# Kernel optimization log

Measured on AMD Instinct MI355X. Metric: run time of the kernel, lower is better.

The kernel has to match this reference:

```python
import jax, jax.numpy as jnp
import numpy as np

N_HEADS = 16
N_KV_HEADS = 4
HEAD_DIM = 64
ROPE_BASE = 10000.0

def _rope_cos_sin(T, dtype):
    # flash-attn style: cos/sin of shape [T, head_dim//2]
    inv_freq = 1.0 / (ROPE_BASE ** (jnp.arange(0, HEAD_DIM, 2, dtype=jnp.float32) / HEAD_DIM))
    freqs = jnp.arange(T, dtype=jnp.float32)[:, None] * inv_freq[None, :]  # [T, D/2]
    return jnp.cos(freqs).astype(dtype), jnp.sin(freqs).astype(dtype)

def _apply_rope(x, cos, sin):
    # x: [B, H, T, D], non-interleaved rotate-half on full head dim
    d2 = HEAD_DIM // 2
    x1, x2 = x[..., :d2], x[..., d2:]
    c = cos[None, None, :, :]
    s = sin[None, None, :, :]
    return jnp.concatenate([x1 * c - x2 * s, x2 * c + x1 * s], axis=-1)

def setup_inputs() -> dict:
    key = jax.random.key(0)
    ks = jax.random.split(key, 6)
    B, T, D = 1, 4096, 1024
    def g(k, shape, scale):
        return jax.random.normal(k, shape, dtype=jnp.float32) * scale
    return {
        "query": g(ks[0], (B, T, D), 1.0),
        "Wq": g(ks[1], (D, D), D ** -0.5),
        "Wk": g(ks[2], (D, N_KV_HEADS * HEAD_DIM), D ** -0.5),
        "Wv": g(ks[3], (D, N_KV_HEADS * HEAD_DIM), D ** -0.5),
        "W1": g(ks[4], (D, 4 * D), D ** -0.5),
        "W2": g(ks[5], (4 * D, D), (4 * D) ** -0.5),
    }

def reference(query, Wq, Wk, Wv, W1, W2):
    B, T, D = query.shape
    # QKV projections -> [B, H, T, Dh]
    q = (query @ Wq).reshape(B, T, N_HEADS, HEAD_DIM).transpose(0, 2, 1, 3)
    k = (query @ Wk).reshape(B, T, N_KV_HEADS, HEAD_DIM).transpose(0, 2, 1, 3)
    v = (query @ Wv).reshape(B, T, N_KV_HEADS, HEAD_DIM).transpose(0, 2, 1, 3)
    # RoPE (seqlen_offset = 0, no cache)
    cos, sin = _rope_cos_sin(T, q.dtype)
    q = _apply_rope(q, cos, sin)
    k = _apply_rope(k, cos, sin)
    # GQA: repeat KV heads to match Q heads
    n_rep = N_HEADS // N_KV_HEADS
    k = jnp.repeat(k, n_rep, axis=1)
    v = jnp.repeat(v, n_rep, axis=1)
    # Scaled dot-product attention, causal
    scale = HEAD_DIM ** -0.5
    scores = jnp.einsum("bhqd,bhkd->bhqk", q, k) * scale
    i = jnp.arange(T)[:, None]
    j = jnp.arange(T)[None, :]
    scores = jnp.where(j > i, jnp.finfo(scores.dtype).min, scores)
    attn = jax.nn.softmax(scores, axis=-1)
    out = jnp.einsum("bhqk,bhkd->bhqd", attn, v)  # [B, H, T, Dh]
    out = out.transpose(0, 2, 1, 3).reshape(B, T, D)
    # out_proj: Linear -> SiLU -> Linear (use_swiglu=True path)
    return jax.nn.silu(out @ W1) @ W2
```

## Files before the change

### kernel.cpp

```cpp
#include <hip/hip_runtime.h>
#include <stdint.h>

typedef unsigned short u16;
typedef __bf16 bf16x8 __attribute__((ext_vector_type(8)));
typedef float f32x4 __attribute__((ext_vector_type(4)));

#define T_SEQ 4096
#define DMODEL 1024

__device__ __forceinline__ float bf2f(u16 x) {
  union { uint32_t u; float f; } v; v.u = ((uint32_t)x) << 16; return v.f;
}
__device__ __forceinline__ u16 f2bf(float f) {
  union { float f; uint32_t u; } v; v.f = f;
  return (u16)((v.u + 0x7FFFu + ((v.u >> 16) & 1u)) >> 16);
}
__device__ __forceinline__ float fexp2(float x) {
#if __has_builtin(__builtin_amdgcn_exp2f)
  return __builtin_amdgcn_exp2f(x);
#else
  return __expf(x * 0.6931471805599453f);
#endif
}
__device__ __forceinline__ uint32_t pack_bf16(float lo, float hi) {
#if __has_builtin(__builtin_amdgcn_cvt_pk_bf16_f32)
  typedef __bf16 bf16x2_t __attribute__((ext_vector_type(2)));
  union { bf16x2_t v; uint32_t u; } c;
  c.v = __builtin_amdgcn_cvt_pk_bf16_f32(lo, hi);
  return c.u;
#else
  union { float f; uint32_t u; } a, b;
  a.f = lo; b.f = hi;
  return __builtin_amdgcn_perm(b.u + 0x8000u, a.u + 0x8000u, 0x07060302u);
#endif
}
__device__ __forceinline__ void async16(void* lds, const void* g) {
  __builtin_amdgcn_global_load_lds(
      (__attribute__((address_space(1))) void*)const_cast<void*>(g),
      (__attribute__((address_space(3))) void*)lds, 16, 0, 0);
}
__device__ __forceinline__ void storeC(u16* C, size_t i, float v) { C[i] = f2bf(v); }
__device__ __forceinline__ void storeC(float* C, size_t i, float v) { C[i] = v; }

__global__ void __launch_bounds__(256) f2b_copy(const float* __restrict__ in,
                                                u16* __restrict__ out, int n) {
  int idx = (blockIdx.x * 256 + threadIdx.x) * 4;
  if (idx >= n) return;
  float4 v = *(const float4*)(in + idx);
  union { u16 s[4]; uint2 q; } b;
  b.s[0] = f2bf(v.x); b.s[1] = f2bf(v.y); b.s[2] = f2bf(v.z); b.s[3] = f2bf(v.w);
  *(uint2*)(out + idx) = b.q;
}

__global__ void __launch_bounds__(256) wtrans(const float* __restrict__ in,
                                              u16* __restrict__ out, int K, int N) {
  __shared__ float tile[64][65];
  const int n0 = blockIdx.x * 64, k0 = blockIdx.y * 64;
  const int tid = threadIdx.x;
  const int r = tid >> 2, c = (tid & 3) * 16;
#pragma unroll
  for (int j = 0; j < 4; ++j) {
    float4 v = *(const float4*)&in[(size_t)(k0 + r) * N + n0 + c + j * 4];
    tile[r][c + j * 4 + 0] = v.x; tile[r][c + j * 4 + 1] = v.y;
    tile[r][c + j * 4 + 2] = v.z; tile[r][c + j * 4 + 3] = v.w;
  }
  __syncthreads();
  union { u16 s[16]; uint4 q[2]; } buf;
#pragma unroll
  for (int j = 0; j < 16; ++j) buf.s[j] = f2bf(tile[c + j][r]);
  u16* dst = out + (size_t)(n0 + r) * K + k0 + c;
  *(uint4*)(dst) = buf.q[0];
  *(uint4*)(dst + 8) = buf.q[1];
}

__global__ void __launch_bounds__(256) vtrans(const u16* __restrict__ qkv,
                                              u16* __restrict__ Vt) {
  __shared__ u16 tile[64][65];
  const int t0 = blockIdx.x * 64, h = blockIdx.y;
  const int tid = threadIdx.x;
  const int r = tid >> 2, q4 = (tid & 3) * 16;
  const u16* src = qkv + (size_t)(t0 + r) * 1536 + 1280 + h * 64 + q4;
  union { u16 s[16]; uint4 q[2]; } buf;
  buf.q[0] = *(const uint4*)(src);
  buf.q[1] = *(const uint4*)(src + 8);
#pragma unroll
  for (int j = 0; j < 16; ++j) tile[r][q4 + j] = buf.s[j];
  __syncthreads();
#pragma unroll
  for (int j = 0; j < 16; ++j) buf.s[j] = tile[q4 + j][r];
  u16* dst = Vt + ((size_t)h * 64 + r) * T_SEQ + t0 + q4;
  *(uint4*)(dst) = buf.q[0];
  *(uint4*)(dst + 8) = buf.q[1];
}

__global__ void __launch_bounds__(256) rope_qk(const u16* __restrict__ qkv,
                                               u16* __restrict__ Q, u16* __restrict__ Ko) {
  const int t = blockIdx.x;
  const int tid = threadIdx.x;
  const int i = tid & 31;
  const float ang = (float)t * powf(10000.f, -(float)i * (1.f / 32.f));
  float s, c;
  sincosf(ang, &s, &c);
  const u16* row = qkv + (size_t)t * 1536;
  const float QS = 0.125f * 1.4426950408889634f;
  const float cq = c * QS, sq = s * QS;
#pragma unroll
  for (int it = 0; it < 2; ++it) {
    int h = (tid >> 5) + it * 8;
    float x1 = bf2f(row[h * 64 + i]);
    float x2 = bf2f(row[h * 64 + 32 + i]);
    size_t o = ((size_t)h * T_SEQ + t) * 64 + i;
    Q[o] = f2bf(x1 * cq - x2 * sq);
    Q[o + 32] = f2bf(x2 * cq + x1 * sq);
  }
  if (tid < 128) {
    int h = tid >> 5;
    float x1 = bf2f(row[1024 + h * 64 + i]);
    float x2 = bf2f(row[1024 + h * 64 + 32 + i]);
    size_t o = ((size_t)h * T_SEQ + t) * 64 + i;
    Ko[o] = f2bf(x1 * c - x2 * s);
    Ko[o + 32] = f2bf(x2 * c + x1 * s);
  }
}

template <int AM, int ACT, typename OutT>
__global__ void __launch_bounds__(256) gemm_bt(const u16* __restrict__ A,
                                               const u16* __restrict__ Bt,
                                               OutT* __restrict__ C,
                                               int M, int N, int K) {
  __shared__ u16 sA[AM * 32][64];
  __shared__ u16 sB[128][64];
  const int tid = threadIdx.x;
  const int w = tid >> 6, lane = tid & 63;
  const int g = lane >> 4, l15 = lane & 15;
  const int r8 = lane >> 3, c8 = lane & 7;
  const int bm = blockIdx.y * (AM * 32), bn = blockIdx.x * 128;

  f32x4 acc[AM][4];
#pragma unroll
  for (int i = 0; i < AM; ++i)
#pragma unroll
    for (int j = 0; j < 4; ++j) acc[i][j] = (f32x4){0.f, 0.f, 0.f, 0.f};

  const u16* Ag = A + (size_t)(bm + w * (AM * 8) + r8) * K + (c8 ^ r8) * 8;
  const u16* Bg = Bt + (size_t)(bn + w * 32 + r8) * K + (c8 ^ r8) * 8;
  const int mrow = (w >> 1) * (AM * 16), ncol = (w & 1) * 64;
  const int swz = l15 & 7;

  for (int k0 = 0; k0 < K; k0 += 64) {
#pragma unroll
    for (int t = 0; t < AM; ++t)
      async16(&sA[w * (AM * 8) + t * 8][0], Ag + (size_t)(t * 8) * K + k0);
#pragma unroll
    for (int t = 0; t < 4; ++t)
      async16(&sB[w * 32 + t * 8][0], Bg + (size_t)(t * 8) * K + k0);
    __syncthreads();
#pragma unroll
    for (int kk = 0; kk < 2; ++kk) {
      const int cb = ((kk * 4 + g) ^ swz) * 8;
      bf16x8 a[AM], b[4];
#pragma unroll
      for (int i = 0; i < AM; ++i) a[i] = *(const bf16x8*)&sA[mrow + i * 16 + l15][cb];
#pragma unroll
      for (int i = 0; i < 4; ++i) b[i] = *(const bf16x8*)&sB[ncol + i * 16 + l15][cb];
#pragma unroll
      for (int mi = 0; mi < AM; ++mi)
#pragma unroll
        for (int ni = 0; ni < 4; ++ni)
          acc[mi][ni] = __builtin_amdgcn_mfma_f32_16x16x32_bf16(a[mi], b[ni], acc[mi][ni], 0, 0, 0);
    }
    __syncthreads();
  }
#pragma unroll
  for (int mi = 0; mi < AM; ++mi)
#pragma unroll
    for (int ni = 0; ni < 4; ++ni)
#pragma unroll
      for (int r = 0; r < 4; ++r) {
        int row = bm + mrow + mi * 16 + g * 4 + r;
        int col = bn + ncol + ni * 16 + l15;
        float v = acc[mi][ni][r];
        if (ACT == 1) v = v / (1.f + __expf(-v));
        storeC(C, (size_t)row * N + col, v);
      }
}

__global__ void __launch_bounds__(256, 2) attn(const u16* __restrict__ Q,
                                               const u16* __restrict__ K,
                                               const u16* __restrict__ Vt,
                                               u16* __restrict__ O0,
                                               u16* __restrict__ O1,
                                               float* __restrict__ L0,
                                               float* __restrict__ L1) {
  __shared__ u16 sK[2][64][64];
  __shared__ u16 sV[2][64][64];
  __shared__ u16 sP[4][64][68];
  const int pr = blockIdx.x >> 1;
  const int split = blockIdx.x & 1;
  const int h = blockIdx.y;
  const int kvh = h >> 2;
  const int tid = threadIdx.x;
  const int w = tid >> 6, lane = tid & 63;
  const int g = lane >> 4, l15 = lane & 15;
  const int r8 = lane >> 3, c8 = lane & 7;
  const int swz = l15 & 7;
  const int t0 = pr, t1 = 31 - pr;
  const int off = split * 64;

  u16* Op = split ? O1 : O0;
  float* Lp = split ? L1 : L0;

  bf16x8 qf[2][2][2];
  {
    const u16* Qh = Q + (size_t)h * T_SEQ * 64;
#pragma unroll
    for (int half = 0; half < 2; ++half)
#pragma unroll
      for (int mi = 0; mi < 2; ++mi) {
        const int q = (half ? t1 : t0) * 128 + w * 32 + mi * 16 + l15;
#pragma unroll
        for (int kk = 0; kk < 2; ++kk)
          qf[half][mi][kk] = *(const bf16x8*)(Qh + (size_t)q * 64 + (kk * 4 + g) * 8);
      }
  }

  f32x4 oacc[2][2][4];
  f32x4 lacc[2][2];
#pragma unroll
  for (int half = 0; half < 2; ++half)
#pragma unroll
    for (int mi = 0; mi < 2; ++mi) {
      lacc[half][mi] = (f32x4){0.f, 0.f, 0.f, 0.f};
#pragma unroll
      for (int nd = 0; nd < 4; ++nd) oacc[half][mi][nd] = (f32x4){0.f, 0.f, 0.f, 0.f};
    }

  bf16x8 ONES;
  {
    union { u16 s[8]; bf16x8 v; } o;
#pragma unroll
    for (int i = 0; i < 8; ++i) o.s[i] = 0x3F80;
    ONES = o.v;
  }

  const u16* Kg = K + ((size_t)kvh * T_SEQ + w * 16 + r8) * 64 + (c8 ^ r8) * 8;
  const u16* Vg = Vt + ((size_t)kvh * 64 + w * 16 + r8) * T_SEQ + (c8 ^ r8) * 8;

#define STAGE(J, B)                                                     \
  {                                                                     \
    const int kv0_ = (J) * 64;                                          \
    async16(&sK[B][w * 16 + 0][0], Kg + (size_t)kv0_ * 64);             \
    async16(&sK[B][w * 16 + 8][0], Kg + (size_t)(kv0_ + 8) * 64);       \
    async16(&sV[B][w * 16 + 0][0], Vg + kv0_);                          \
    async16(&sV[B][w * 16 + 8][0], Vg + (size_t)8 * T_SEQ + kv0_);      \
  }

#define BODY(B, ACT0, M0, M1)                                                     \
  {                                                                               \
    const int b_ = (B);                                                           \
    f32x4 s1[2][4], s0[2][4];                                                     \
    _Pragma("unroll") for (int mi = 0; mi < 2; ++mi)                              \
    _Pragma("unroll") for (int kt = 0; kt < 4; ++kt) {                            \
      s1[mi][kt] = (f32x4){0.f, 0.f, 0.f, 0.f};                                   \
      if (ACT0) s0[mi][kt] = (f32x4){0.f, 0.f, 0.f, 0.f};                         \
    }                                                                             \
    _Pragma("unroll") for (int kt = 0; kt < 4; ++kt)                              \
    _Pragma("unroll") for (int kk = 0; kk < 2; ++kk) {                            \
      bf16x8 kf = *(const bf16x8*)&sK[b_][kt * 16 + l15][((kk * 4 + g) ^ swz) * 8]; \
      _Pragma("unroll") for (int mi = 0; mi < 2; ++mi) {                          \
        s1[mi][kt] = __builtin_amdgcn_mfma_f32_16x16x32_bf16(kf, qf[1][mi][kk], s1[mi][kt], 0, 0, 0); \
        if (ACT0)                                                                 \
          s0[mi][kt] = __builtin_amdgcn_mfma_f32_16x16x32_bf16(kf, qf[0][mi][kk], s0[mi][kt], 0, 0, 0); \
      }                                                                           \
    }                                                                             \
    _Pragma("unroll") for (int mi = 0; mi < 2; ++mi) {                            \
      const int thr_ = w * 32 + mi * 16 + l15 - off;                              \
      _Pragma("unroll") for (int kt = 0; kt < 4; ++kt) {                          \
        float p_[4];                                                              \
        _Pragma("unroll") for (int r = 0; r < 4; ++r) {                           \
          float p = fexp2(s1[mi][kt][r]);                                         \
          if (M1 && (kt * 16 + g * 4 + r > thr_)) p = 0.f;                        \
          p_[r] = p;                                                              \
        }                                                                         \
        uint2 pk;                                                                 \
        pk.x = pack_bf16(p_[0], p_[1]);                                           \
        pk.y = pack_bf16(p_[2], p_[3]);                                           \
        *(uint2*)&sP[w][32 + mi * 16 + l15][kt * 16 + g * 4] = pk;                \
      }                                                                           \
      if (ACT0) {                                                                 \
        _Pragma("unroll") for (int kt = 0; kt < 4; ++kt) {                        \
          float p_[4];                                                            \
          _Pragma("unroll") for (int r = 0; r < 4; ++r) {                         \
            float p = fexp2(s0[mi][kt][r]);                                       \
            if (M0 && (kt * 16 + g * 4 + r > thr_)) p = 0.f;                      \
            p_[r] = p;                                                            \
          }                                                                       \
          uint2 pk;                                                               \
          pk.x = pack_bf16(p_[0], p_[1]);                                         \
          pk.y = pack_bf16(p_[2], p_[3]);                                         \
          *(uint2*)&sP[w][mi * 16 + l15][kt * 16 + g * 4] = pk;                   \
        }                                                                         \
      }                                                                           \
    }                                                                             \
    __builtin_amdgcn_wave_barrier();          \
    _Pragma("unroll") for (int kk = 0; kk < 2; ++kk) {                            \
      bf16x8 pf1[2], pf0[2];                                                      \
      _Pragma("unroll") for (int mi = 0; mi < 2; ++mi) {                          \
        pf1[mi] = *(const bf16x8*)&sP[w][32 + mi * 16 + l15][kk * 32 + g * 8];    \
        if (ACT0) pf0[mi] = *(const bf16x8*)&sP[w][mi * 16 + l15][kk * 32 + g * 8]; \
      }                                                                           \
      _Pragma("unroll") for (int mi = 0; mi < 2; ++mi) {                          \
        lacc[1][mi] = __builtin_amdgcn_mfma_f32_16x16x32_bf16(pf1[mi], ONES, lacc[1][mi], 0, 0, 0); \
        if (ACT0)                                                                 \
          lacc[0][mi] = __builtin_amdgcn_mfma_f32_16x16x32_bf16(pf0[mi], ONES, lacc[0][mi], 0, 0, 0); \
      }                                                                           \
      _Pragma("unroll") for (int nd = 0; nd < 4; ++nd) {                          \
        bf16x8 vf = *(const bf16x8*)&sV[b_][nd * 16 + l15][((kk * 4 + g) ^ swz) * 8]; \
        _Pragma("unroll") for (int mi = 0; mi < 2; ++mi) {                        \
          oacc[1][mi][nd] = __builtin_amdgcn_mfma_f32_16x16x32_bf16(pf1[mi], vf, oacc[1][mi][nd], 0, 0, 0); \
          if (ACT0)                                                               \
            oacc[0][mi][nd] = __builtin_amdgcn_mfma_f32_16x16x32_bf16(pf0[mi], vf, oacc[0][mi][nd], 0, 0, 0); \
        }                                                                         \
      }                                                                           \
    }                                                                             \
  }

  const int e0 = 2 * t0 + split, e1 = 2 * t1 + split;
  STAGE(split, 0);
  int jj = split, b = 0;
  for (; jj < e0; jj += 2, b ^= 1) {
    __syncthreads();
    STAGE(jj + 2, b ^ 1);
    BODY(b, true, false, false);
  }
  {
    __syncthreads();
    STAGE(jj + 2, b ^ 1);
    BODY(b, true, true, false);
    jj += 2; b ^= 1;
  }
  for (; jj < e1; jj += 2, b ^= 1) {
    __syncthreads();
    STAGE(jj + 2, b ^ 1);
    BODY(b, false, false, false);
  }
  {
    __syncthreads();
    BODY(b, false, false, true);
  }
#undef STAGE
#undef BODY

#pragma unroll
  for (int half = 0; half < 2; ++half) {
    const int tb = (half ? t1 : t0) * 128;
#pragma unroll
    for (int mi = 0; mi < 2; ++mi)
#pragma unroll
      for (int r = 0; r < 4; ++r) {
        const int trow = tb + w * 32 + mi * 16 + g * 4 + r;
#pragma unroll
        for (int nd = 0; nd < 4; ++nd)
          Op[(size_t)trow * DMODEL + h * 64 + nd * 16 + l15] = f2bf(oacc[half][mi][nd][r]);
        if (l15 == 0) Lp[h * T_SEQ + trow] = lacc[half][mi][r];
      }
  }
}

__global__ void __launch_bounds__(256) attn_combine(const u16* __restrict__ O0,
                                                    const u16* __restrict__ O1,
                                                    const float* __restrict__ L0,
                                                    const float* __restrict__ L1,
                                                    u16* __restrict__ AO) {
  const int t = blockIdx.x, tid = threadIdx.x;
  const int h = tid >> 4, d4 = (tid & 15) * 4;
  const float inv = 1.f / (L0[h * T_SEQ + t] + L1[h * T_SEQ + t]);
  const size_t idx = (size_t)t * DMODEL + h * 64 + d4;
  union { uint2 q; u16 s[4]; } a, b, o;
  a.q = *(const uint2*)(O0 + idx);
  b.q = *(const uint2*)(O1 + idx);
#pragma unroll
  for (int i = 0; i < 4; ++i) o.s[i] = f2bf((bf2f(a.s[i]) + bf2f(b.s[i])) * inv);
  *(uint2*)(AO + idx) = o.q;
}

extern "C" void kernel_launch(void* const* d_in, const int* in_sizes, int n_in,
                              void* d_out, int out_size, void* d_ws, size_t ws_size,
                              hipStream_t stream) {
  const float* query = (const float*)d_in[0];
  const float* Wq = (const float*)d_in[1];
  const float* Wk = (const float*)d_in[2];
  const float* Wv = (const float*)d_in[3];
  const float* W1 = (const float*)d_in[4];
  const float* W2 = (const float*)d_in[5];
  float* out = (float*)d_out;

  char* ws = (char*)d_ws;
  size_t off = 0;
  auto alloc = [&](size_t bytes) { char* p = ws + off; off += (bytes + 255) & ~(size_t)255; return p; };
  u16* Xb   = (u16*)alloc((size_t)4096 * 1024 * 2);
  u16* QKVb = (u16*)alloc((size_t)4096 * 1536 * 2);
  u16* Qb   = (u16*)alloc((size_t)16 * 4096 * 64 * 2);
  u16* Kb   = (u16*)alloc((size_t)4 * 4096 * 64 * 2);
  u16* Vtb  = (u16*)alloc((size_t)4 * 4096 * 64 * 2);
  u16* H    = (u16*)ws;
  u16*   O0p = Xb;
  u16*   O1p = QKVb;
  float* L0p = (float*)(QKVb + (size_t)4096 * 1024);
  float* L1p = L0p + 16 * T_SEQ;
  u16* WqkvT = (u16*)alloc((size_t)1536 * 1024 * 2);
  u16* W1T   = (u16*)alloc((size_t)4096 * 1024 * 2);
  u16* W2T   = (u16*)alloc((size_t)1024 * 4096 * 2);
  u16* AO    = (u16*)alloc((size_t)4096 * 1024 * 2);
  (void)ws_size; (void)in_sizes; (void)n_in; (void)out_size;

  f2b_copy<<<4096, 256, 0, stream>>>(query, Xb, 4096 * 1024);
  wtrans<<<dim3(16, 16), 256, 0, stream>>>(Wq, WqkvT, 1024, 1024);
  wtrans<<<dim3(4, 16), 256, 0, stream>>>(Wk, WqkvT + (size_t)1024 * 1024, 1024, 256);
  wtrans<<<dim3(4, 16), 256, 0, stream>>>(Wv, WqkvT + (size_t)1280 * 1024, 1024, 256);
  wtrans<<<dim3(64, 16), 256, 0, stream>>>(W1, W1T, 1024, 4096);
  wtrans<<<dim3(16, 64), 256, 0, stream>>>(W2, W2T, 4096, 1024);

  gemm_bt<2, 0, u16><<<dim3(12, 64), 256, 0, stream>>>(Xb, WqkvT, QKVb, 4096, 1536, 1024);
  rope_qk<<<4096, 256, 0, stream>>>(QKVb, Qb, Kb);
  vtrans<<<dim3(64, 4), 256, 0, stream>>>(QKVb, Vtb);
  attn<<<dim3(32, 16), 256, 0, stream>>>(Qb, Kb, Vtb, O0p, O1p, L0p, L1p);
  attn_combine<<<4096, 256, 0, stream>>>(O0p, O1p, L0p, L1p, AO);
  gemm_bt<4, 1, u16><<<dim3(32, 32), 256, 0, stream>>>(AO, W1T, H, 4096, 4096, 1024);
  gemm_bt<2, 0, float><<<dim3(8, 64), 256, 0, stream>>>(H, W2T, out, 4096, 1024, 4096);
}
```

Baseline: 318.0 us.

## Merge prep launches and split-K the final W2 GEMM with combine pass

Folds the input conversion and five weight-transpose launches into one prep kernel, and merges RoPE with the V transpose into one launch, to cut launch overhead and tail gaps. The final K=4096 GEMM becomes a 128x128-tile split-K kernel over two K halves. The first half writes fp32 to the output and the second writes bf16 partials into the now-free W1T buffer, and a combine kernel adds them. This raises block count and parallelism for the narrow N=1024 GEMM. The cost is an extra pass over the output and bf16 rounding of half the partial sum.

```diff
diff --git a/kernel.cpp b/kernel.cpp
--- a/kernel.cpp
+++ b/kernel.cpp
@@ -42,21 +42,11 @@
 __device__ __forceinline__ void storeC(u16* C, size_t i, float v) { C[i] = f2bf(v); }
 __device__ __forceinline__ void storeC(float* C, size_t i, float v) { C[i] = v; }
 
-__global__ void __launch_bounds__(256) f2b_copy(const float* __restrict__ in,
-                                                u16* __restrict__ out, int n) {
-  int idx = (blockIdx.x * 256 + threadIdx.x) * 4;
-  if (idx >= n) return;
-  float4 v = *(const float4*)(in + idx);
-  union { u16 s[4]; uint2 q; } b;
-  b.s[0] = f2bf(v.x); b.s[1] = f2bf(v.y); b.s[2] = f2bf(v.z); b.s[3] = f2bf(v.w);
-  *(uint2*)(out + idx) = b.q;
-}
-
-__global__ void __launch_bounds__(256) wtrans(const float* __restrict__ in,
-                                              u16* __restrict__ out, int K, int N) {
-  __shared__ float tile[64][65];
-  const int n0 = blockIdx.x * 64, k0 = blockIdx.y * 64;
-  const int tid = threadIdx.x;
+__device__ __forceinline__ void wtrans_body(const float* __restrict__ in,
+                                            u16* __restrict__ out, int K, int N,
+                                            int bx, int by, int tid,
+                                            float (*tile)[65]) {
+  const int n0 = bx * 64, k0 = by * 64;
   const int r = tid >> 2, c = (tid & 3) * 16;
 #pragma unroll
   for (int j = 0; j < 4; ++j) {
@@ -73,53 +63,90 @@
   *(uint4*)(dst + 8) = buf.q[1];
 }
 
-__global__ void __launch_bounds__(256) vtrans(const u16* __restrict__ qkv,
-                                              u16* __restrict__ Vt) {
+__global__ void __launch_bounds__(256) prep(const float* __restrict__ query,
+                                            const float* __restrict__ Wq,
+                                            const float* __restrict__ Wk,
+                                            const float* __restrict__ Wv,
+                                            const float* __restrict__ W1,
+                                            const float* __restrict__ W2,
+                                            u16* __restrict__ Xb,
+                                            u16* __restrict__ WqkvT,
+                                            u16* __restrict__ W1T,
+                                            u16* __restrict__ W2T) {
+  __shared__ float tile[64][65];
+  const int b = blockIdx.x, tid = threadIdx.x;
+  if (b < 4096) {
+    int idx = (b * 256 + tid) * 4;
+    float4 v = *(const float4*)(query + idx);
+    union { u16 s[4]; uint2 q; } o;
+    o.s[0] = f2bf(v.x); o.s[1] = f2bf(v.y); o.s[2] = f2bf(v.z); o.s[3] = f2bf(v.w);
+    *(uint2*)(Xb + idx) = o.q;
+  } else if (b < 4352) {
+    int t = b - 4096;
+    wtrans_body(Wq, WqkvT, 1024, 1024, t & 15, t >> 4, tid, tile);
+  } else if (b < 4416) {
+    int t = b - 4352;
+    wtrans_body(Wk, WqkvT + (size_t)1024 * 1024, 1024, 256, t & 3, t >> 2, tid, tile);
+  } else if (b < 4480) {
+    int t = b - 4416;
+    wtrans_body(Wv, WqkvT + (size_t)1280 * 1024, 1024, 256, t & 3, t >> 2, tid, tile);
+  } else if (b < 5504) {
+    int t = b - 4480;
+    wtrans_body(W1, W1T, 1024, 4096, t & 63, t >> 6, tid, tile);
+  } else {
+    int t = b - 5504;
+    wtrans_body(W2, W2T, 4096, 1024, t & 15, t >> 4, tid, tile);
+  }
+}
+
+__global__ void __launch_bounds__(256) rope_vt(const u16* __restrict__ qkv,
+                                               u16* __restrict__ Q,
+                                               u16* __restrict__ Ko,
+                                               u16* __restrict__ Vt) {
   __shared__ u16 tile[64][65];
-  const int t0 = blockIdx.x * 64, h = blockIdx.y;
-  const int tid = threadIdx.x;
-  const int r = tid >> 2, q4 = (tid & 3) * 16;
-  const u16* src = qkv + (size_t)(t0 + r) * 1536 + 1280 + h * 64 + q4;
-  union { u16 s[16]; uint4 q[2]; } buf;
-  buf.q[0] = *(const uint4*)(src);
-  buf.q[1] = *(const uint4*)(src + 8);
-#pragma unroll
-  for (int j = 0; j < 16; ++j) tile[r][q4 + j] = buf.s[j];
-  __syncthreads();
-#pragma unroll
-  for (int j = 0; j < 16; ++j) buf.s[j] = tile[q4 + j][r];
-  u16* dst = Vt + ((size_t)h * 64 + r) * T_SEQ + t0 + q4;
-  *(uint4*)(dst) = buf.q[0];
-  *(uint4*)(dst + 8) = buf.q[1];
-}
-
-__global__ void __launch_bounds__(256) rope_qk(const u16* __restrict__ qkv,
-                                               u16* __restrict__ Q, u16* __restrict__ Ko) {
-  const int t = blockIdx.x;
-  const int tid = threadIdx.x;
-  const int i = tid & 31;
-  const float ang = (float)t * powf(10000.f, -(float)i * (1.f / 32.f));
-  float s, c;
-  sincosf(ang, &s, &c);
-  const u16* row = qkv + (size_t)t * 1536;
-  const float QS = 0.125f * 1.4426950408889634f;
-  const float cq = c * QS, sq = s * QS;
-#pragma unroll
-  for (int it = 0; it < 2; ++it) {
-    int h = (tid >> 5) + it * 8;
-    float x1 = bf2f(row[h * 64 + i]);
-    float x2 = bf2f(row[h * 64 + 32 + i]);
-    size_t o = ((size_t)h * T_SEQ + t) * 64 + i;
-    Q[o] = f2bf(x1 * cq - x2 * sq);
-    Q[o + 32] = f2bf(x2 * cq + x1 * sq);
-  }
-  if (tid < 128) {
-    int h = tid >> 5;
-    float x1 = bf2f(row[1024 + h * 64 + i]);
-    float x2 = bf2f(row[1024 + h * 64 + 32 + i]);
-    size_t o = ((size_t)h * T_SEQ + t) * 64 + i;
-    Ko[o] = f2bf(x1 * c - x2 * s);
-    Ko[o + 32] = f2bf(x2 * c + x1 * s);
+  const int b = blockIdx.x, tid = threadIdx.x;
+  if (b < 4096) {
+    const int t = b;
+    const int i = tid & 31;
+    const float ang = (float)t * powf(10000.f, -(float)i * (1.f / 32.f));
+    float s, c;
+    sincosf(ang, &s, &c);
+    const u16* row = qkv + (size_t)t * 1536;
+    const float QS = 0.125f * 1.4426950408889634f;
+    const float cq = c * QS, sq = s * QS;
+#pragma unroll
+    for (int it = 0; it < 2; ++it) {
+      int h = (tid >> 5) + it * 8;
+      float x1 = bf2f(row[h * 64 + i]);
+      float x2 = bf2f(row[h * 64 + 32 + i]);
+      size_t o = ((size_t)h * T_SEQ + t) * 64 + i;
+      Q[o] = f2bf(x1 * cq - x2 * sq);
+      Q[o + 32] = f2bf(x2 * cq + x1 * sq);
+    }
+    if (tid < 128) {
+      int h = tid >> 5;
+      float x1 = bf2f(row[1024 + h * 64 + i]);
+      float x2 = bf2f(row[1024 + h * 64 + 32 + i]);
+      size_t o = ((size_t)h * T_SEQ + t) * 64 + i;
+      Ko[o] = f2bf(x1 * c - x2 * s);
+      Ko[o + 32] = f2bf(x2 * c + x1 * s);
+    }
+  } else {
+    const int t = b - 4096;
+    const int t0 = (t & 63) * 64, h = t >> 6;
+    const int r = tid >> 2, q4 = (tid & 3) * 16;
+    const u16* src = qkv + (size_t)(t0 + r) * 1536 + 1280 + h * 64 + q4;
+    union { u16 s[16]; uint4 q[2]; } buf;
+    buf.q[0] = *(const uint4*)(src);
+    buf.q[1] = *(const uint4*)(src + 8);
+#pragma unroll
+    for (int j = 0; j < 16; ++j) tile[r][q4 + j] = buf.s[j];
+    __syncthreads();
+#pragma unroll
+    for (int j = 0; j < 16; ++j) buf.s[j] = tile[q4 + j][r];
+    u16* dst = Vt + ((size_t)h * 64 + r) * T_SEQ + t0 + q4;
+    *(uint4*)(dst) = buf.q[0];
+    *(uint4*)(dst + 8) = buf.q[1];
   }
 }
 
@@ -183,6 +210,78 @@
         if (ACT == 1) v = v / (1.f + __expf(-v));
         storeC(C, (size_t)row * N + col, v);
       }
+}
+
+__global__ void __launch_bounds__(256, 2) gemm_w2(const u16* __restrict__ A,
+                                                  const u16* __restrict__ Bt,
+                                                  float* __restrict__ C0,
+                                                  u16* __restrict__ C1) {
+  __shared__ u16 sA[128][64];
+  __shared__ u16 sB[128][64];
+  const int K = 4096, N = 1024;
+  const int z = blockIdx.z, koff = z * 2048;
+  const int tid = threadIdx.x;
+  const int w = tid >> 6, lane = tid & 63;
+  const int g = lane >> 4, l15 = lane & 15;
+  const int r8 = lane >> 3, c8 = lane & 7;
+  const int bm = blockIdx.y * 128, bn = blockIdx.x * 128;
+
+  f32x4 acc[4][4];
+#pragma unroll
+  for (int i = 0; i < 4; ++i)
+#pragma unroll
+    for (int j = 0; j < 4; ++j) acc[i][j] = (f32x4){0.f, 0.f, 0.f, 0.f};
+
+  const u16* Ag = A + (size_t)(bm + w * 32 + r8) * K + koff + (c8 ^ r8) * 8;
+  const u16* Bg = Bt + (size_t)(bn + w * 32 + r8) * K + koff + (c8 ^ r8) * 8;
+  const int mrow = (w >> 1) * 64, ncol = (w & 1) * 64;
+  const int swz = l15 & 7;
+
+  for (int k0 = 0; k0 < 2048; k0 += 64) {
+#pragma unroll
+    for (int t = 0; t < 4; ++t) {
+      async16(&sA[w * 32 + t * 8][0], Ag + (size_t)(t * 8) * K + k0);
+      async16(&sB[w * 32 + t * 8][0], Bg + (size_t)(t * 8) * K + k0);
+    }
+    __syncthreads();
+#pragma unroll
+    for (int kk = 0; kk < 2; ++kk) {
+      const int cb = ((kk * 4 + g) ^ swz) * 8;
+      bf16x8 a[4], b[4];
+#pragma unroll
+      for (int i = 0; i < 4; ++i) {
+        a[i] = *(const bf16x8*)&sA[mrow + i * 16 + l15][cb];
+        b[i] = *(const bf16x8*)&sB[ncol + i * 16 + l15][cb];
+      }
+#pragma unroll
+      for (int mi = 0; mi < 4; ++mi)
+#pragma unroll
+        for (int ni = 0; ni < 4; ++ni)
+          acc[mi][ni] = __builtin_amdgcn_mfma_f32_16x16x32_bf16(a[mi], b[ni], acc[mi][ni], 0, 0, 0);
+    }
+    __syncthreads();
+  }
+#pragma unroll
+  for (int mi = 0; mi < 4; ++mi)
+#pragma unroll
+    for (int ni = 0; ni < 4; ++ni)
+#pragma unroll
+      for (int r = 0; r < 4; ++r) {
+        size_t idx = (size_t)(bm + mrow + mi * 16 + g * 4 + r) * N + bn + ncol + ni * 16 + l15;
+        if (z == 0) C0[idx] = acc[mi][ni][r];
+        else        C1[idx] = f2bf(acc[mi][ni][r]);
+      }
+}
+
+__global__ void __launch_bounds__(256) w2_combine(float* __restrict__ out,
+                                                  const u16* __restrict__ P1) {
+  int idx = (blockIdx.x * 256 + threadIdx.x) * 4;
+  float4 v = *(const float4*)(out + idx);
+  union { uint2 q; u16 s[4]; } p;
+  p.q = *(const uint2*)(P1 + idx);
+  v.x += bf2f(p.s[0]); v.y += bf2f(p.s[1]);
+  v.z += bf2f(p.s[2]); v.w += bf2f(p.s[3]);
+  *(float4*)(out + idx) = v;
 }
 
 __global__ void __launch_bounds__(256, 2) attn(const u16* __restrict__ Q,
@@ -412,20 +511,15 @@
   u16* W1T   = (u16*)alloc((size_t)4096 * 1024 * 2);
   u16* W2T   = (u16*)alloc((size_t)1024 * 4096 * 2);
   u16* AO    = (u16*)alloc((size_t)4096 * 1024 * 2);
+  u16* P1    = W1T;
   (void)ws_size; (void)in_sizes; (void)n_in; (void)out_size;
 
-  f2b_copy<<<4096, 256, 0, stream>>>(query, Xb, 4096 * 1024);
-  wtrans<<<dim3(16, 16), 256, 0, stream>>>(Wq, WqkvT, 1024, 1024);
-  wtrans<<<dim3(4, 16), 256, 0, stream>>>(Wk, WqkvT + (size_t)1024 * 1024, 1024, 256);
-  wtrans<<<dim3(4, 16), 256, 0, stream>>>(Wv, WqkvT + (size_t)1280 * 1024, 1024, 256);
-  wtrans<<<dim3(64, 16), 256, 0, stream>>>(W1, W1T, 1024, 4096);
-  wtrans<<<dim3(16, 64), 256, 0, stream>>>(W2, W2T, 4096, 1024);
-
+  prep<<<6528, 256, 0, stream>>>(query, Wq, Wk, Wv, W1, W2, Xb, WqkvT, W1T, W2T);
   gemm_bt<2, 0, u16><<<dim3(12, 64), 256, 0, stream>>>(Xb, WqkvT, QKVb, 4096, 1536, 1024);
-  rope_qk<<<4096, 256, 0, stream>>>(QKVb, Qb, Kb);
-  vtrans<<<dim3(64, 4), 256, 0, stream>>>(QKVb, Vtb);
+  rope_vt<<<4352, 256, 0, stream>>>(QKVb, Qb, Kb, Vtb);
   attn<<<dim3(32, 16), 256, 0, stream>>>(Qb, Kb, Vtb, O0p, O1p, L0p, L1p);
   attn_combine<<<4096, 256, 0, stream>>>(O0p, O1p, L0p, L1p, AO);
   gemm_bt<4, 1, u16><<<dim3(32, 32), 256, 0, stream>>>(AO, W1T, H, 4096, 4096, 1024);
-  gemm_bt<2, 0, float><<<dim3(8, 64), 256, 0, stream>>>(H, W2T, out, 4096, 1024, 4096);
-}
+  gemm_w2<<<dim3(8, 32, 2), 256, 0, stream>>>(H, W2T, out, P1);
+  w2_combine<<<4096, 256, 0, stream>>>(out, P1);
+}
```

Measured after the change: 291.7 us. 1.09x faster.
